# Kernel optimization log

Measured on AMD Instinct MI355X. Metric: run time of the kernel, lower is better.

## Reference

```python
import jax, jax.numpy as jnp
import numpy as np

N_NODES = 100000
N_EDGES = 1600000
IN_CH = 64
HID_CH = 64
NUM_LAYERS = 3


def _init_linear(key, out_ch, in_ch, bias=True):
    # torch nn.Linear default init: U(-1/sqrt(in), 1/sqrt(in))
    bound = 1.0 / np.sqrt(in_ch)
    kw, kb = jax.random.split(key)
    W = jax.random.uniform(kw, (out_ch, in_ch), jnp.float32, -bound, bound)
    if bias:
        b = jax.random.uniform(kb, (out_ch,), jnp.float32, -bound, bound)
        return W, b
    return W, None


def setup_inputs() -> dict:
    key = jax.random.key(0)
    ks = jax.random.split(key, 8)
    x = jax.random.normal(ks[0], (N_NODES, IN_CH), jnp.float32)
    edge_index = jax.random.randint(ks[1], (2, N_EDGES), 0, N_NODES, jnp.int64)
    inp = {"x": x, "edge_index": edge_index}
    in_dims = [IN_CH] + [HID_CH] * (NUM_LAYERS - 1)
    for i, d_in in enumerate(in_dims):
        kl, kr = jax.random.split(ks[2 + i])
        Wl, bl = _init_linear(kl, HID_CH, d_in, bias=True)   # lin_l: aggregated neighbors (has bias)
        Wr, _ = _init_linear(kr, HID_CH, d_in, bias=False)   # lin_r: root/self features (no bias)
        inp[f"Wl{i}"] = Wl
        inp[f"bl{i}"] = bl
        inp[f"Wr{i}"] = Wr
    return inp


def _sage_conv(x, src, dst, deg_inv, Wl, bl, Wr):
    # mean aggregation of source features into destination nodes
    msg = x[src]                                              # [E, d]  (irregular gather)
    agg = jax.ops.segment_sum(msg, dst, num_segments=N_NODES)  # [N, d] (irregular scatter)
    agg = agg * deg_inv[:, None]
    return agg @ Wl.T + bl + x @ Wr.T


def reference(x, edge_index, Wl0, bl0, Wr0, Wl1, bl1, Wr1, Wl2, bl2, Wr2):
    src, dst = edge_index[0], edge_index[1]
    deg = jax.ops.segment_sum(jnp.ones((N_EDGES,), x.dtype), dst, num_segments=N_NODES)
    deg_inv = 1.0 / jnp.maximum(deg, 1.0)
    params = [(Wl0, bl0, Wr0), (Wl1, bl1, Wr1), (Wl2, bl2, Wr2)]
    h = x
    for i, (Wl, bl, Wr) in enumerate(params):
        h = _sage_conv(h, src, dst, deg_inv, Wl, bl, Wr)
        if i < NUM_LAYERS - 1:
            h = jax.nn.relu(h)  # dropout is identity in eval mode
    return h
```

## Files before the change

### kernel.cpp

```cpp
#include <hip/hip_runtime.h>
#include <hip/hip_bf16.h>

#define N_NODES 100000
#define N_EDGES 1600000
#define CH 64


__device__ __forceinline__ unsigned short f2bf(float f) {
    unsigned int u = __float_as_uint(f);
    u += 0x7FFF + ((u >> 16) & 1);
    return (unsigned short)(u >> 16);
}
__device__ __forceinline__ float bf2f(unsigned short b) {
    return __uint_as_float(((unsigned int)b) << 16);
}


__global__ void k_hist(const int* __restrict__ dst, int* __restrict__ cnt, int E) {
    int i = blockIdx.x * blockDim.x + threadIdx.x;
    int E4 = E >> 2;
    if (i < E4) {
        int4 d = ((const int4*)dst)[i];
        atomicAdd(&cnt[d.x], 1);
        atomicAdd(&cnt[d.y], 1);
        atomicAdd(&cnt[d.z], 1);
        atomicAdd(&cnt[d.w], 1);
    }
    if (i == 0) for (int e = E4 * 4; e < E; ++e) atomicAdd(&cnt[dst[e]], 1);
}

__global__ __launch_bounds__(1024) void k_scanA(const int* __restrict__ cnt, int N,
                                                int* __restrict__ rowp, int* __restrict__ bsum) {
    __shared__ int s[1024];
    int t = threadIdx.x;
    int g = blockIdx.x * 1024 + t;
    int v = (g < N) ? cnt[g] : 0;
    s[t] = v;
    __syncthreads();
    for (int off = 1; off < 1024; off <<= 1) {
        int x = (t >= off) ? s[t - off] : 0;
        __syncthreads();
        s[t] += x;
        __syncthreads();
    }
    if (g < N) rowp[g] = s[t] - v;
    if (t == 1023) bsum[blockIdx.x] = s[1023];
}

__global__ __launch_bounds__(1024) void k_scanB(int* __restrict__ bsum, int nb) {
    __shared__ int s[1024];
    int t = threadIdx.x;
    int v = (t < nb) ? bsum[t] : 0;
    s[t] = v;
    __syncthreads();
    for (int off = 1; off < 1024; off <<= 1) {
        int x = (t >= off) ? s[t - off] : 0;
        __syncthreads();
        s[t] += x;
        __syncthreads();
    }
    if (t < nb) bsum[t] = s[t] - v;
}

__global__ void k_scanC(int* __restrict__ rowp, const int* __restrict__ cnt,
                        const int* __restrict__ bsum, int* __restrict__ cursor,
                        float* __restrict__ dinv, int N) {
    int g = blockIdx.x * blockDim.x + threadIdx.x;
    if (g < N) {
        int r = rowp[g] + bsum[g >> 10];
        rowp[g]   = r;
        cursor[g] = r;
        int d = cnt[g];
        dinv[g] = 1.0f / (float)(d > 1 ? d : 1);
    }
}

__global__ void k_fill(const int* __restrict__ src, const int* __restrict__ dst,
                       int* __restrict__ cursor, int* __restrict__ col, int E) {
    int i = blockIdx.x * blockDim.x + threadIdx.x;
    int E4 = E >> 2;
    if (i < E4) {
        int4 s = ((const int4*)src)[i];
        int4 d = ((const int4*)dst)[i];
        col[atomicAdd(&cursor[d.x], 1)] = s.x;
        col[atomicAdd(&cursor[d.y], 1)] = s.y;
        col[atomicAdd(&cursor[d.z], 1)] = s.z;
        col[atomicAdd(&cursor[d.w], 1)] = s.w;
    }
    if (i == 0) for (int e = E4 * 4; e < E; ++e)
        col[atomicAdd(&cursor[dst[e]], 1)] = src[e];
}

__global__ __launch_bounds__(256) void k_transform(const float* __restrict__ h,
                                                   const float* __restrict__ Wl,
                                                   const float* __restrict__ bl,
                                                   const float* __restrict__ Wr,
                                                   unsigned short* __restrict__ T,
                                                   float* __restrict__ S, int N) {
    int lane = threadIdx.x & 63;
    float wl[CH], wr[CH];
    const float4* Wl4 = (const float4*)(Wl + lane * CH);
    const float4* Wr4 = (const float4*)(Wr + lane * CH);
#pragma unroll
    for (int q = 0; q < CH / 4; ++q) {
        float4 a = Wl4[q];
        wl[4 * q] = a.x; wl[4 * q + 1] = a.y; wl[4 * q + 2] = a.z; wl[4 * q + 3] = a.w;
        float4 b = Wr4[q];
        wr[4 * q] = b.x; wr[4 * q + 1] = b.y; wr[4 * q + 2] = b.z; wr[4 * q + 3] = b.w;
    }
    float bias = bl[lane];

    int wid    = (blockIdx.x * blockDim.x + threadIdx.x) >> 6;
    int nwaves = (gridDim.x * blockDim.x) >> 6;
    for (int n = wid; n < N; n += nwaves) {
        float hv = h[n * CH + lane];
        float ol = 0.f, orr = 0.f;
#pragma unroll
        for (int c = 0; c < CH; ++c) {
            float hc = __uint_as_float(__builtin_amdgcn_readlane(__float_as_uint(hv), c));
            ol  += hc * wl[c];
            orr += hc * wr[c];
        }
        T[n * CH + lane] = f2bf(ol);
        S[n * CH + lane] = orr + bias;
    }
}

__global__ __launch_bounds__(256) void k_gather(const unsigned short* __restrict__ T,
                                                const float* __restrict__ S,
                                                const int* __restrict__ rowp,
                                                const int* __restrict__ cnt,
                                                const float* __restrict__ dinv,
                                                const int* __restrict__ col,
                                                float* __restrict__ out,
                                                int relu, int N) {
    int wave = threadIdx.x >> 6, lane = threadIdx.x & 63;
    int n = blockIdx.x * 4 + wave;
    if (n >= N) return;

    int start = rowp[n];
    int deg   = cnt[n];

    float a0 = 0.f, a1 = 0.f, a2 = 0.f, a3 = 0.f;
    int e = 0;
    for (; e + 4 <= deg; e += 4) {
        int s0 = col[start + e];
        int s1 = col[start + e + 1];
        int s2 = col[start + e + 2];
        int s3 = col[start + e + 3];
        a0 += bf2f(T[s0 * CH + lane]);
        a1 += bf2f(T[s1 * CH + lane]);
        a2 += bf2f(T[s2 * CH + lane]);
        a3 += bf2f(T[s3 * CH + lane]);
    }
    for (; e < deg; ++e) a0 += bf2f(T[col[start + e] * CH + lane]);

    float o = S[n * CH + lane] + ((a0 + a1) + (a2 + a3)) * dinv[n];
    if (relu) o = fmaxf(o, 0.f);
    out[n * CH + lane] = o;
}


extern "C" void kernel_launch(void* const* d_in, const int* in_sizes, int n_in,
                              void* d_out, int out_size, void* d_ws, size_t ws_size,
                              hipStream_t stream) {
    const float* x   = (const float*)d_in[0];
    const int*   ei  = (const int*)d_in[1];
    const int E = in_sizes[1] / 2;
    const int N = in_sizes[0] / CH;
    const int* src = ei;
    const int* dst = ei + E;

    const float* Wl[3] = { (const float*)d_in[2], (const float*)d_in[5], (const float*)d_in[8] };
    const float* bl[3] = { (const float*)d_in[3], (const float*)d_in[6], (const float*)d_in[9] };
    const float* Wr[3] = { (const float*)d_in[4], (const float*)d_in[7], (const float*)d_in[10] };

    char* ws = (char*)d_ws;
    size_t off = 0;
    auto take = [&](size_t bytes) { char* p = ws + off; off += (bytes + 255) & ~(size_t)255; return p; };
    int*            cnt    = (int*)           take((size_t)N * 4);
    int*            rowp   = (int*)           take((size_t)(N + 1) * 4);
    int*            cursor = (int*)           take((size_t)N * 4);
    float*          dinv   = (float*)         take((size_t)N * 4);
    int*            bsum   = (int*)           take(4096);
    int*            col    = (int*)           take((size_t)E * 4);
    unsigned short* T      = (unsigned short*)take((size_t)N * CH * 2);
    float*          S      = (float*)         take((size_t)N * CH * 4);
    float*          buf0   = (float*)         take((size_t)N * CH * 4);
    float*          outp   = (float*)d_out;

    hipMemsetAsync(cnt, 0, (size_t)N * 4, stream);

    int tb = 256;
    int E4 = E >> 2;
    k_hist<<<(E4 + tb - 1) / tb, tb, 0, stream>>>(dst, cnt, E);

    int nb = (N + 1023) / 1024;
    k_scanA<<<nb, 1024, 0, stream>>>(cnt, N, rowp, bsum);
    k_scanB<<<1, 1024, 0, stream>>>(bsum, nb);
    k_scanC<<<(N + tb - 1) / tb, tb, 0, stream>>>(rowp, cnt, bsum, cursor, dinv, N);
    k_fill<<<(E4 + tb - 1) / tb, tb, 0, stream>>>(src, dst, cursor, col, E);

    int gblocks = (N + 3) / 4;
    k_transform<<<1024, 256, 0, stream>>>(x, Wl[0], bl[0], Wr[0], T, S, N);
    k_gather<<<gblocks, 256, 0, stream>>>(T, S, rowp, cnt, dinv, col, buf0, 1, N);
    k_transform<<<1024, 256, 0, stream>>>(buf0, Wl[1], bl[1], Wr[1], T, S, N);
    k_gather<<<gblocks, 256, 0, stream>>>(T, S, rowp, cnt, dinv, col, buf0, 1, N);
    k_transform<<<1024, 256, 0, stream>>>(buf0, Wl[2], bl[2], Wr[2], T, S, N);
    k_gather<<<gblocks, 256, 0, stream>>>(T, S, rowp, cnt, dinv, col, outp, 0, N);
}
```

Measured before the change: 646.9 us.

## Pack bf16 pairs in gather with half-wave edge split; multi-pass CSR fill

The gather kernel now has each half-wave process a different neighbor edge, with each lane loading two packed bf16 values in one 32-bit load, then combines the halves with a cross-lane shuffle. This doubles the edges in flight per wave and widens the per-lane loads. The CSR fill kernel is split into 8 passes over destination ranges to localize the atomic cursor updates and col writes. That costs re-reading the edge arrays 8 times.

Result: faster. 581.9 us (-10.0%).

```diff
diff --git a/kernel.cpp b/kernel.cpp
--- a/kernel.cpp
+++ b/kernel.cpp
@@ -4,6 +4,7 @@
 #define N_NODES 100000
 #define N_EDGES 1600000
 #define CH 64
+#define NPASS 8
 
 
 __device__ __forceinline__ unsigned short f2bf(float f) {
@@ -75,19 +76,26 @@
     }
 }
 
-__global__ void k_fill(const int* __restrict__ src, const int* __restrict__ dst,
-                       int* __restrict__ cursor, int* __restrict__ col, int E) {
-    int i = blockIdx.x * blockDim.x + threadIdx.x;
+__global__ __launch_bounds__(256) void k_fill(const int* __restrict__ src,
+                                              const int* __restrict__ dst,
+                                              int* __restrict__ cursor,
+                                              int* __restrict__ col, int E, int N) {
     int E4 = E >> 2;
-    if (i < E4) {
-        int4 s = ((const int4*)src)[i];
-        int4 d = ((const int4*)dst)[i];
-        col[atomicAdd(&cursor[d.x], 1)] = s.x;
-        col[atomicAdd(&cursor[d.y], 1)] = s.y;
-        col[atomicAdd(&cursor[d.z], 1)] = s.z;
-        col[atomicAdd(&cursor[d.w], 1)] = s.w;
-    }
-    if (i == 0) for (int e = E4 * 4; e < E; ++e)
+    int tid = blockIdx.x * blockDim.x + threadIdx.x;
+    int nth = gridDim.x * blockDim.x;
+    int span = (N + NPASS - 1) / NPASS;
+    for (int p = 0; p < NPASS; ++p) {
+        int lo = p * span, hi = lo + span;
+        for (int i = tid; i < E4; i += nth) {
+            int4 d = ((const int4*)dst)[i];
+            int4 s = ((const int4*)src)[i];
+            if (d.x >= lo && d.x < hi) col[atomicAdd(&cursor[d.x], 1)] = s.x;
+            if (d.y >= lo && d.y < hi) col[atomicAdd(&cursor[d.y], 1)] = s.y;
+            if (d.z >= lo && d.z < hi) col[atomicAdd(&cursor[d.z], 1)] = s.z;
+            if (d.w >= lo && d.w < hi) col[atomicAdd(&cursor[d.w], 1)] = s.w;
+        }
+    }
+    if (tid == 0) for (int e = E4 * 4; e < E; ++e)
         col[atomicAdd(&cursor[dst[e]], 1)] = src[e];
 }
 
@@ -135,29 +143,51 @@
                                                 float* __restrict__ out,
                                                 int relu, int N) {
     int wave = threadIdx.x >> 6, lane = threadIdx.x & 63;
+    int half = lane >> 5, li = lane & 31;
     int n = blockIdx.x * 4 + wave;
     if (n >= N) return;
 
     int start = rowp[n];
     int deg   = cnt[n];
-
-    float a0 = 0.f, a1 = 0.f, a2 = 0.f, a3 = 0.f;
+    const int* cp = col + start;
+
+    float a0 = 0.f, a1 = 0.f, b0 = 0.f, b1 = 0.f;
+    float c0 = 0.f, c1 = 0.f, d0 = 0.f, d1 = 0.f;
     int e = 0;
-    for (; e + 4 <= deg; e += 4) {
-        int s0 = col[start + e];
-        int s1 = col[start + e + 1];
-        int s2 = col[start + e + 2];
-        int s3 = col[start + e + 3];
-        a0 += bf2f(T[s0 * CH + lane]);
-        a1 += bf2f(T[s1 * CH + lane]);
-        a2 += bf2f(T[s2 * CH + lane]);
-        a3 += bf2f(T[s3 * CH + lane]);
-    }
-    for (; e < deg; ++e) a0 += bf2f(T[col[start + e] * CH + lane]);
-
-    float o = S[n * CH + lane] + ((a0 + a1) + (a2 + a3)) * dinv[n];
-    if (relu) o = fmaxf(o, 0.f);
-    out[n * CH + lane] = o;
+    for (; e + 8 <= deg; e += 8) {
+        int s0 = cp[e + 0 + half];
+        int s1 = cp[e + 2 + half];
+        int s2 = cp[e + 4 + half];
+        int s3 = cp[e + 6 + half];
+        unsigned u0 = *(const unsigned*)(T + (size_t)s0 * CH + 2 * li);
+        unsigned u1 = *(const unsigned*)(T + (size_t)s1 * CH + 2 * li);
+        unsigned u2 = *(const unsigned*)(T + (size_t)s2 * CH + 2 * li);
+        unsigned u3 = *(const unsigned*)(T + (size_t)s3 * CH + 2 * li);
+        a0 += bf2f((unsigned short)u0); a1 += bf2f((unsigned short)(u0 >> 16));
+        b0 += bf2f((unsigned short)u1); b1 += bf2f((unsigned short)(u1 >> 16));
+        c0 += bf2f((unsigned short)u2); c1 += bf2f((unsigned short)(u2 >> 16));
+        d0 += bf2f((unsigned short)u3); d1 += bf2f((unsigned short)(u3 >> 16));
+    }
+    for (; e < deg; e += 2) {
+        if (e + half < deg) {
+            int s = cp[e + half];
+            unsigned u = *(const unsigned*)(T + (size_t)s * CH + 2 * li);
+            a0 += bf2f((unsigned short)u); a1 += bf2f((unsigned short)(u >> 16));
+        }
+    }
+    float r0 = (a0 + b0) + (c0 + d0);
+    float r1 = (a1 + b1) + (c1 + d1);
+    r0 += __shfl(r0, lane ^ 32, 64);
+    r1 += __shfl(r1, lane ^ 32, 64);
+
+    if (half == 0) {
+        float dv = dinv[n];
+        float2 sv = *(const float2*)(S + (size_t)n * CH + 2 * li);
+        float o0 = sv.x + r0 * dv;
+        float o1 = sv.y + r1 * dv;
+        if (relu) { o0 = fmaxf(o0, 0.f); o1 = fmaxf(o1, 0.f); }
+        *(float2*)(out + (size_t)n * CH + 2 * li) = make_float2(o0, o1);
+    }
 }
 
 
@@ -199,7 +229,9 @@
     k_scanA<<<nb, 1024, 0, stream>>>(cnt, N, rowp, bsum);
     k_scanB<<<1, 1024, 0, stream>>>(bsum, nb);
     k_scanC<<<(N + tb - 1) / tb, tb, 0, stream>>>(rowp, cnt, bsum, cursor, dinv, N);
-    k_fill<<<(E4 + tb - 1) / tb, tb, 0, stream>>>(src, dst, cursor, col, E);
+
+    int fblocks = (E4 + tb - 1) / tb;
+    k_fill<<<fblocks, tb, 0, stream>>>(src, dst, cursor, col, E, N);
 
     int gblocks = (N + 3) / 4;
     k_transform<<<1024, 256, 0, stream>>>(x, Wl[0], bl[0], Wr[0], T, S, N);
```
